# Kernel optimization log

Hardware: AMD Instinct MI355X
Metric: run time of the kernel (lower is better)

Reference implementation:

```python
import jax, jax.numpy as jnp
import numpy as np

N = 100000      # nodes
E = 3200000     # edges (avg degree 32)
DIN, DH, DOUT = 256, 256, 64
K = 10          # propagation hops


def _uniform(key, shape, fan_in):
    b = 1.0 / np.sqrt(fan_in)
    return jax.random.uniform(key, shape, jnp.float32, -b, b)


def setup_inputs() -> dict:
    key = jax.random.key(0)
    ks = jax.random.split(key, 8)
    x = jax.random.normal(ks[0], (N, DIN), jnp.float32)
    edge_index = jax.random.randint(ks[1], (2, E), 0, N, dtype=jnp.int64)
    W1 = _uniform(ks[2], (DIN, DH), DIN)
    b1 = _uniform(ks[3], (DH,), DIN)
    W2 = _uniform(ks[4], (DH, DOUT), DH)
    b2 = _uniform(ks[5], (DOUT,), DH)
    proj_w = _uniform(ks[6], (DOUT,), DOUT)
    proj_b = _uniform(ks[7], (), DOUT)
    return {"x": x, "edge_index": edge_index, "W1": W1, "b1": b1,
            "W2": W2, "b2": b2, "proj_w": proj_w, "proj_b": proj_b}


def _gcn_norm(edge_index, num_nodes):
    # add self-loops with weight 1, symmetric normalization deg^-1/2 A deg^-1/2
    loops = jnp.arange(num_nodes, dtype=edge_index.dtype)
    row = jnp.concatenate([edge_index[0], loops])
    col = jnp.concatenate([edge_index[1], loops])
    w = jnp.ones(row.shape[0], jnp.float32)
    deg = jax.ops.segment_sum(w, col, num_segments=num_nodes)
    dinv = jnp.where(deg > 0, jax.lax.rsqrt(deg), 0.0)
    norm = dinv[row] * dinv[col]  # edge weight is 1
    return row, col, norm


def reference(x, edge_index, W1, b1, W2, b2, proj_w, proj_b):
    h = jax.nn.relu(x @ W1 + b1)
    h = h @ W2 + b2                               # [N, DOUT]
    row, col, norm = _gcn_norm(edge_index, N)
    preds = [h]
    for _ in range(K):
        h = jax.ops.segment_sum(norm[:, None] * h[row], col, num_segments=N)
        preds.append(h)
    pps = jnp.stack(preds, axis=1)                # [N, K+1, DOUT]
    score = jax.nn.sigmoid(pps @ proj_w + proj_b) # [N, K+1]
    out = jnp.einsum('nk,nkc->nc', score, pps)    # adaptive hop pooling
    return out
```

## Files before the change

kernel.cpp:

```cpp
#include <hip/hip_runtime.h>
#include <hip/hip_bf16.h>
#include <math.h>


#define WAVE 64
#define NBLK 1024
#define RS 520

__device__ inline float bf2f(unsigned short u) {
    union { unsigned int i; float f; } v; v.i = ((unsigned int)u) << 16; return v.f;
}
__device__ inline unsigned short f2bf(float f) {
    __hip_bfloat16 b = __float2bfloat16(f);
    union { __hip_bfloat16 b; unsigned short u; } v; v.b = b; return v.u;
}
__device__ inline float bflo(unsigned u) {
    union { unsigned i; float f; } v; v.i = u << 16; return v.f;
}
__device__ inline float bfhi(unsigned u) {
    union { unsigned i; float f; } v; v.i = u & 0xffff0000u; return v.f;
}

typedef __attribute__((ext_vector_type(8))) short bf16x8;
typedef __attribute__((ext_vector_type(16))) float f32x16;

__global__ void detect_kernel(const unsigned* __restrict__ e, int* __restrict__ sflag) {
    __shared__ int any;
    if (threadIdx.x == 0) any = 0;
    __syncthreads();
    unsigned nz = 0;
    int t = threadIdx.x;
    for (int i = 0; i < 8; ++i) nz |= e[(size_t)(t * 8 + i) * 2 + 1];
    if (nz) atomicOr(&any, 1);
    __syncthreads();
    if (t == 0) *sflag = any ? 1 : 2;
}

__global__ void passA_kernel(const int* __restrict__ eidx, const int* __restrict__ sflag,
                             int* __restrict__ blk_cnt, int E, int NB, int EPB) {
    __shared__ int lh[512];
    int t = threadIdx.x, blk = blockIdx.x;
    for (int i = t; i < NB; i += 256) lh[i] = 0;
    __syncthreads();
    int s = *sflag;
    int base = blk * EPB;
    int end = base + EPB; if (end > E) end = E;
    for (int e = base + t; e < end; e += 256) {
        int c = eidx[(size_t)s * (size_t)(E + e)];
        atomicAdd(&lh[c >> 8], 1);
    }
    __syncthreads();
    for (int i = t; i < NB; i += 256)
        blk_cnt[(size_t)blk * NB + i] = lh[i];
}

__global__ void scan1_kernel(const int* __restrict__ in, int* __restrict__ out,
                             int* __restrict__ bsums, int n) {
    __shared__ int s[256];
    int t = threadIdx.x;
    int idx = blockIdx.x * 1024 + t * 4;
    int x0 = (idx + 0 < n) ? in[idx + 0] : 0;
    int x1 = (idx + 1 < n) ? in[idx + 1] : 0;
    int x2 = (idx + 2 < n) ? in[idx + 2] : 0;
    int x3 = (idx + 3 < n) ? in[idx + 3] : 0;
    int lsum = x0 + x1 + x2 + x3;
    s[t] = lsum;
    __syncthreads();
    for (int o = 1; o < 256; o <<= 1) {
        int v = (t >= o) ? s[t - o] : 0;
        __syncthreads();
        if (t >= o) s[t] += v;
        __syncthreads();
    }
    int excl = s[t] - lsum;
    if (idx + 0 < n) out[idx + 0] = excl;
    if (idx + 1 < n) out[idx + 1] = excl + x0;
    if (idx + 2 < n) out[idx + 2] = excl + x0 + x1;
    if (idx + 3 < n) out[idx + 3] = excl + x0 + x1 + x2;
    if (t == 255) bsums[blockIdx.x] = s[255];
}

__global__ void scan2g_kernel(int* __restrict__ bsums, int nb) {
    __shared__ int part[256];
    int t = threadIdx.x;
    int v[4]; int run = 0;
    #pragma unroll
    for (int j = 0; j < 4; ++j) {
        int i = t * 4 + j;
        int x = (i < nb) ? bsums[i] : 0;
        v[j] = run; run += x;
    }
    part[t] = run;
    __syncthreads();
    for (int o = 1; o < 256; o <<= 1) {
        int x = (t >= o) ? part[t - o] : 0;
        __syncthreads();
        if (t >= o) part[t] += x;
        __syncthreads();
    }
    int excl = part[t] - run;
    #pragma unroll
    for (int j = 0; j < 4; ++j) {
        int i = t * 4 + j;
        if (i < nb) bsums[i] = excl + v[j];
    }
}

__global__ void scan3_kernel(int* __restrict__ arr, const int* __restrict__ bsums,
                             int n, int total) {
    int t = threadIdx.x;
    int idx = blockIdx.x * 1024 + t * 4;
    int add = bsums[blockIdx.x];
    #pragma unroll
    for (int i = 0; i < 4; ++i)
        if (idx + i < n) arr[idx + i] += add;
    if (blockIdx.x == 0 && t == 0) arr[n] = total;
}

__global__ void passB_kernel(const int* __restrict__ eidx, const int* __restrict__ sflag,
                             const int* __restrict__ pbase, int2* __restrict__ pairs,
                             int E, int NB, int EPB) {
    __shared__ int lcur[512];
    int t = threadIdx.x, blk = blockIdx.x;
    for (int i = t; i < NB; i += 256) lcur[i] = pbase[(size_t)blk * NB + i];
    __syncthreads();
    int s = *sflag;
    int base = blk * EPB;
    int end = base + EPB; if (end > E) end = E;
    for (int e = base + t; e < end; e += 256) {
        int r = eidx[(size_t)s * (size_t)e];
        int c = eidx[(size_t)s * (size_t)(E + e)];
        int pos = atomicAdd(&lcur[c >> 8], 1);
        pairs[pos] = make_int2(r, c);
    }
}

__global__ void passD_kernel(const int2* __restrict__ pairs, const int* __restrict__ pbase,
                             int* __restrict__ cnt, int N, int NB) {
    __shared__ int lcnt[256];
    int b = blockIdx.x, t = threadIdx.x;
    lcnt[t] = 0;
    __syncthreads();
    for (int blk = t; blk < NBLK; blk += 256) {
        int w0 = pbase[(size_t)blk * NB + b];
        int w1 = pbase[(size_t)blk * NB + b + 1];
        for (int i = w0; i < w1; ++i)
            atomicAdd(&lcnt[pairs[i].y & 255], 1);
    }
    __syncthreads();
    int node = b * 256 + t;
    if (node < N) cnt[node] = lcnt[t];
}

__global__ void dinv_kernel(const int* __restrict__ cnt, float* __restrict__ dinv, int n) {
    int i = blockIdx.x * blockDim.x + threadIdx.x;
    if (i < n) dinv[i] = rsqrtf((float)(cnt[i] + 1));
}

__global__ void passC_kernel(const int2* __restrict__ pairs, const int* __restrict__ pbase,
                             const int* __restrict__ offs, int* __restrict__ csr_src,
                             int N, int NB) {
    __shared__ int lcur[256];
    int b = blockIdx.x, t = threadIdx.x;
    int node = b * 256 + t;
    lcur[t] = (node < N) ? offs[node] : 0;
    __syncthreads();
    for (int blk = t; blk < NBLK; blk += 256) {
        int w0 = pbase[(size_t)blk * NB + b];
        int w1 = pbase[(size_t)blk * NB + b + 1];
        for (int i = w0; i < w1; ++i) {
            int2 p = pairs[i];
            int pos = atomicAdd(&lcur[p.y & 255], 1);
            csr_src[pos] = p.x;
        }
    }
}

__global__ void wconv_kernel(const float* __restrict__ W, unsigned short* __restrict__ Wf,
                             int K, int Nn) {
    int i = blockIdx.x * blockDim.x + threadIdx.x;
    if (i >= K * Nn) return;
    int k = i / Nn, n = i - k * Nn;
    Wf[(size_t)(k >> 3) * Nn * 8 + n * 8 + (k & 7)] = f2bf(W[i]);
}

__global__ __launch_bounds__(256, 4) void mlp_fused(
        const float* __restrict__ x,
        const unsigned short* __restrict__ W1f,
        const float* __restrict__ b1,
        const unsigned short* __restrict__ W2f,
        const float* __restrict__ b2,
        const float* __restrict__ dinv,
        const float* __restrict__ pw, const float* __restrict__ pb,
        float* __restrict__ out, unsigned short* __restrict__ g,
        int M) {
    __shared__ unsigned short xfrag[4 * RS];
    __shared__ unsigned short h1frag[32 * RS];
    __shared__ float pools[2][2][2][16];

    int tid = threadIdx.x;
    int wave = tid >> 6, lane = tid & 63;
    int half = lane >> 5, l31 = lane & 31;
    int rt = wave & 1;
    int cw = wave >> 1;
    int bm = blockIdx.x * 64;

    f32x16 acc1[4] = {};

    float4 xv[2];
    #pragma unroll
    for (int i = 0; i < 2; ++i) {
        int f = i * 256 + tid;
        int row = f >> 3, c4 = (f & 7) * 4;
        int grow = bm + row;
        xv[i] = (grow < M) ? *(const float4*)(x + (size_t)grow * 256 + c4)
                           : make_float4(0.f, 0.f, 0.f, 0.f);
    }

    for (int it = 0; it < 8; ++it) {
        #pragma unroll
        for (int i = 0; i < 2; ++i) {
            int f = i * 256 + tid;
            int row = f >> 3, c4 = (f & 7) * 4;
            int region = c4 >> 3, off = c4 & 7;
            ushort4 u;
            u.x = f2bf(xv[i].x); u.y = f2bf(xv[i].y);
            u.z = f2bf(xv[i].z); u.w = f2bf(xv[i].w);
            *(ushort4*)&xfrag[region * RS + row * 8 + off] = u;
        }
        __syncthreads();
        if (it < 7) {
            int k0 = (it + 1) * 32;
            #pragma unroll
            for (int i = 0; i < 2; ++i) {
                int f = i * 256 + tid;
                int row = f >> 3, c4 = (f & 7) * 4;
                int grow = bm + row;
                xv[i] = (grow < M) ? *(const float4*)(x + (size_t)grow * 256 + k0 + c4)
                                   : make_float4(0.f, 0.f, 0.f, 0.f);
            }
        }
        #pragma unroll
        for (int s = 0; s < 2; ++s) {
            int region = it * 4 + s * 2 + half;
            bf16x8 a = *(bf16x8*)&xfrag[(s * 2 + half) * RS + (rt * 32 + l31) * 8];
            #pragma unroll
            for (int j = 0; j < 4; ++j) {
                int ch = cw * 128 + j * 32 + l31;
                bf16x8 b = *(const bf16x8*)(W1f + (size_t)region * 2048 + ch * 8);
                acc1[j] = __builtin_amdgcn_mfma_f32_32x32x16_bf16(a, b, acc1[j], 0, 0, 0);
            }
        }
        __syncthreads();
    }

    #pragma unroll
    for (int j = 0; j < 4; ++j) {
        int ch = cw * 128 + j * 32 + l31;
        float bb = b1[ch];
        int region = ch >> 3, off = ch & 7;
        #pragma unroll
        for (int reg = 0; reg < 16; ++reg) {
            int rowin = (reg & 3) + 8 * (reg >> 2) + 4 * half;
            int row = rt * 32 + rowin;
            float v = fmaxf(acc1[j][reg] + bb, 0.f);
            h1frag[region * RS + row * 8 + off] = f2bf(v);
        }
    }
    __syncthreads();

    int rt2 = wave >> 1, ct2 = wave & 1;
    f32x16 acc2 = {};
    #pragma unroll
    for (int s = 0; s < 16; ++s) {
        bf16x8 a = *(bf16x8*)&h1frag[(s * 2 + half) * RS + (rt2 * 32 + l31) * 8];
        bf16x8 b = *(const bf16x8*)(W2f + (size_t)(s * 2 + half) * 512 + (ct2 * 32 + l31) * 8);
        acc2 = __builtin_amdgcn_mfma_f32_32x32x16_bf16(a, b, acc2, 0, 0, 0);
    }

    float bb = b2[ct2 * 32 + l31];
    float pwv = pw[ct2 * 32 + l31];
    float pbv = pb[0];
    float hreg[16];
    #pragma unroll
    for (int reg = 0; reg < 16; ++reg) {
        float h = acc2[reg] + bb;
        hreg[reg] = h;
        float d = h * pwv;
        d += __shfl_xor(d, 1, 64);
        d += __shfl_xor(d, 2, 64);
        d += __shfl_xor(d, 4, 64);
        d += __shfl_xor(d, 8, 64);
        d += __shfl_xor(d, 16, 64);
        if (l31 == 0) pools[rt2][ct2][half][reg] = d;
    }
    __syncthreads();
    #pragma unroll
    for (int reg = 0; reg < 16; ++reg) {
        int rowin = (reg & 3) + 8 * (reg >> 2) + 4 * half;
        int row = bm + rt2 * 32 + rowin;
        float d = pools[rt2][0][half][reg] + pools[rt2][1][half][reg];
        float sg = 1.f / (1.f + __expf(-(d + pbv)));
        float h = hreg[reg];
        if (row < M) {
            float dv = dinv[row];
            out[(size_t)row * 64 + ct2 * 32 + l31] = sg * h;
            g[(size_t)row * 64 + ct2 * 32 + l31]   = f2bf(dv * h);
        }
    }
}

__global__ void spmm_kernel(const int* __restrict__ offs, const int* __restrict__ src,
                            const float* __restrict__ dinv,
                            const unsigned* __restrict__ gin,
                            unsigned short* __restrict__ gout,
                            float* __restrict__ out,
                            const float* __restrict__ pw, const float* __restrict__ pb,
                            int n) {
    int wid = (blockIdx.x * blockDim.x + threadIdx.x) >> 6;
    int lane = threadIdx.x & 63;
    if (wid >= n) return;
    int g = lane >> 4;
    int q = lane & 15;
    int c = __builtin_amdgcn_readfirstlane(wid);
    int e0   = __builtin_amdgcn_readfirstlane(offs[c]);
    int eend = __builtin_amdgcn_readfirstlane(offs[c + 1]);

    float a0 = 0.f, a1 = 0.f, a2 = 0.f, a3 = 0.f;
    for (int e = e0; e < eend; e += 32) {
        #pragma unroll
        for (int i = 0; i < 8; ++i) {
            int ei = e + i * 4 + g;
            int ec = (ei < eend) ? ei : (eend - 1);
            float m = (ei < eend) ? 1.f : 0.f;
            int s = src[ec];
            uint2 v = *(const uint2*)(gin + (size_t)s * 32 + q * 2);
            a0 = fmaf(m, bflo(v.x), a0);
            a1 = fmaf(m, bfhi(v.x), a1);
            a2 = fmaf(m, bflo(v.y), a2);
            a3 = fmaf(m, bfhi(v.y), a3);
        }
    }

    a0 += __shfl_xor(a0, 16, 64); a0 += __shfl_xor(a0, 32, 64);
    a1 += __shfl_xor(a1, 16, 64); a1 += __shfl_xor(a1, 32, 64);
    a2 += __shfl_xor(a2, 16, 64); a2 += __shfl_xor(a2, 32, 64);
    a3 += __shfl_xor(a3, 16, 64); a3 += __shfl_xor(a3, 32, 64);

    uint2 sv = *(const uint2*)(gin + (size_t)c * 32 + q * 2);
    a0 += bflo(sv.x); a1 += bfhi(sv.x);
    a2 += bflo(sv.y); a3 += bfhi(sv.y);

    float dc = dinv[c];
    float h0 = dc * a0, h1 = dc * a1, h2 = dc * a2, h3 = dc * a3;

    float4 pv = *(const float4*)(pw + q * 4);
    float d = h0 * pv.x + h1 * pv.y + h2 * pv.z + h3 * pv.w;
    d += __shfl_xor(d, 1, 64);
    d += __shfl_xor(d, 2, 64);
    d += __shfl_xor(d, 4, 64);
    d += __shfl_xor(d, 8, 64);
    float sg = 1.f / (1.f + __expf(-(d + pb[0])));

    if (g == 0) {
        ushort4 gw;
        gw.x = f2bf(dc * h0); gw.y = f2bf(dc * h1);
        gw.z = f2bf(dc * h2); gw.w = f2bf(dc * h3);
        *(ushort4*)(gout + (size_t)c * 64 + q * 4) = gw;
        float4 o = *(float4*)(out + (size_t)c * 64 + q * 4);
        o.x += sg * h0; o.y += sg * h1; o.z += sg * h2; o.w += sg * h3;
        *(float4*)(out + (size_t)c * 64 + q * 4) = o;
    }
}

extern "C" void kernel_launch(void* const* d_in, const int* in_sizes, int n_in,
                              void* d_out, int out_size, void* d_ws, size_t ws_size,
                              hipStream_t stream) {
    const float* x  = (const float*)d_in[0];
    const int* eidx = (const int*)d_in[1];
    const float* W1 = (const float*)d_in[2];
    const float* b1 = (const float*)d_in[3];
    const float* W2 = (const float*)d_in[4];
    const float* b2 = (const float*)d_in[5];
    const float* pw = (const float*)d_in[6];
    const float* pb = (const float*)d_in[7];
    float* out = (float*)d_out;

    const int N = in_sizes[0] / 256;
    const int E = in_sizes[1] / 2;
    const int NB = (N + 255) >> 8;
    const int EPB = (E + NBLK - 1) / NBLK;
    const int M = NB * NBLK;

    size_t woff = 0;
    auto alloc = [&](size_t bytes) -> void* {
        void* p = (char*)d_ws + woff;
        woff += (bytes + 255) & ~(size_t)255;
        return p;
    };
    int*   sflag   = (int*)alloc(4);
    int*   cnt     = (int*)alloc((size_t)N * 4);
    float* dinv    = (float*)alloc((size_t)N * 4);
    int*   offs    = (int*)alloc(((size_t)N + 1) * 4);
    int*   bsums   = (int*)alloc(1024 * 4);
    int*   bsums2  = (int*)alloc(1024 * 4);
    int*   pbase   = (int*)alloc(((size_t)M + 1) * 4);
    int*   csr_src = (int*)alloc((size_t)E * 4);
    int2*  pairs   = (int2*)alloc((size_t)E * 8);
    unsigned short* W1f = (unsigned short*)alloc((size_t)256 * 256 * 2);
    unsigned short* W2f = (unsigned short*)alloc((size_t)64 * 256 * 2);
    unsigned short* gA = (unsigned short*)alloc((size_t)N * 64 * 2);
    unsigned short* gB = (unsigned short*)alloc((size_t)N * 64 * 2);

    detect_kernel<<<1, 256, 0, stream>>>((const unsigned*)eidx, sflag);

    passA_kernel<<<NBLK, 256, 0, stream>>>(eidx, sflag, pbase, E, NB, EPB);
    int nb2 = (M + 1023) / 1024;
    scan1_kernel<<<nb2, 256, 0, stream>>>(pbase, pbase, bsums2, M);
    scan2g_kernel<<<1, 256, 0, stream>>>(bsums2, nb2);
    scan3_kernel<<<nb2, 256, 0, stream>>>(pbase, bsums2, M, E);
    passB_kernel<<<NBLK, 256, 0, stream>>>(eidx, sflag, pbase, pairs, E, NB, EPB);
    passD_kernel<<<NB, 256, 0, stream>>>(pairs, pbase, cnt, N, NB);
    dinv_kernel<<<(N + 255) / 256, 256, 0, stream>>>(cnt, dinv, N);
    int nb1 = (N + 1023) / 1024;
    scan1_kernel<<<nb1, 256, 0, stream>>>(cnt, offs, bsums, N);
    scan2g_kernel<<<1, 256, 0, stream>>>(bsums, nb1);
    scan3_kernel<<<nb1, 256, 0, stream>>>(offs, bsums, N, E);
    passC_kernel<<<NB, 256, 0, stream>>>(pairs, pbase, offs, csr_src, N, NB);

    wconv_kernel<<<(256 * 256 + 255) / 256, 256, 0, stream>>>(W1, W1f, 256, 256);
    wconv_kernel<<<(64 * 256 + 255) / 256, 256, 0, stream>>>(W2, W2f, 256, 64);
    int gb = (N + 63) / 64;
    mlp_fused<<<gb, 256, 0, stream>>>(x, W1f, b1, W2f, b2, dinv, pw, pb,
                                      out, gA, N);

    int nwb = (N + 3) / 4;
    unsigned short* gin = gA;
    unsigned short* gout = gB;
    for (int k = 0; k < 10; ++k) {
        spmm_kernel<<<nwb, 256, 0, stream>>>(offs, csr_src, dinv,
                                             (const unsigned*)gin, gout, out, pw, pb, N);
        unsigned short* t = gin; gin = gout; gout = t;
    }
}
```

Baseline: 980.3 us.

## Fuse ten SpMM hops into one persistent cooperative kernel with grid sync

Replaces the ten per-hop SpMM launches with a single cooperative persistent kernel. Each wave handles a contiguous chunk of destination nodes across all hops and ping-pongs between two bf16 buffers, with a grid-wide barrier between hops. It also folds the dinv computation into passD, removing one launch. The aim is to cut launch overhead and inter-kernel gaps. In exchange, occupancy is limited to the cooperative grid size, and the grid barriers plus fixed node-to-wave assignment can cause load imbalance.

After: 3.458 ms. 253% more time.

```diff
diff --git a/kernel.cpp b/kernel.cpp
--- a/kernel.cpp
+++ b/kernel.cpp
@@ -1,6 +1,9 @@
 #include <hip/hip_runtime.h>
 #include <hip/hip_bf16.h>
+#include <hip/hip_cooperative_groups.h>
 #include <math.h>
+
+namespace cg = cooperative_groups;
 
 
 #define WAVE 64
@@ -136,7 +139,8 @@
 }
 
 __global__ void passD_kernel(const int2* __restrict__ pairs, const int* __restrict__ pbase,
-                             int* __restrict__ cnt, int N, int NB) {
+                             int* __restrict__ cnt, float* __restrict__ dinv,
+                             int N, int NB) {
     __shared__ int lcnt[256];
     int b = blockIdx.x, t = threadIdx.x;
     lcnt[t] = 0;
@@ -149,12 +153,10 @@
     }
     __syncthreads();
     int node = b * 256 + t;
-    if (node < N) cnt[node] = lcnt[t];
-}
-
-__global__ void dinv_kernel(const int* __restrict__ cnt, float* __restrict__ dinv, int n) {
-    int i = blockIdx.x * blockDim.x + threadIdx.x;
-    if (i < n) dinv[i] = rsqrtf((float)(cnt[i] + 1));
+    if (node < N) {
+        cnt[node] = lcnt[t];
+        dinv[node] = rsqrtf((float)(lcnt[t] + 1));
+    }
 }
 
 __global__ void passC_kernel(const int2* __restrict__ pairs, const int* __restrict__ pbase,
@@ -310,66 +312,79 @@
     }
 }
 
-__global__ void spmm_kernel(const int* __restrict__ offs, const int* __restrict__ src,
-                            const float* __restrict__ dinv,
-                            const unsigned* __restrict__ gin,
-                            unsigned short* __restrict__ gout,
-                            float* __restrict__ out,
-                            const float* __restrict__ pw, const float* __restrict__ pb,
-                            int n) {
-    int wid = (blockIdx.x * blockDim.x + threadIdx.x) >> 6;
+__global__ __launch_bounds__(256) void spmm_coop(
+        const int* __restrict__ offs, const int* __restrict__ src,
+        const float* __restrict__ dinv,
+        unsigned* __restrict__ gA, unsigned* __restrict__ gB,
+        float* __restrict__ out,
+        const float* __restrict__ pw, const float* __restrict__ pb,
+        int n, int dpw) {
+    cg::grid_group grid = cg::this_grid();
+    int gw = (blockIdx.x * blockDim.x + threadIdx.x) >> 6;
     int lane = threadIdx.x & 63;
-    if (wid >= n) return;
     int g = lane >> 4;
     int q = lane & 15;
-    int c = __builtin_amdgcn_readfirstlane(wid);
-    int e0   = __builtin_amdgcn_readfirstlane(offs[c]);
-    int eend = __builtin_amdgcn_readfirstlane(offs[c + 1]);
-
-    float a0 = 0.f, a1 = 0.f, a2 = 0.f, a3 = 0.f;
-    for (int e = e0; e < eend; e += 32) {
-        #pragma unroll
-        for (int i = 0; i < 8; ++i) {
-            int ei = e + i * 4 + g;
-            int ec = (ei < eend) ? ei : (eend - 1);
-            float m = (ei < eend) ? 1.f : 0.f;
-            int s = src[ec];
-            uint2 v = *(const uint2*)(gin + (size_t)s * 32 + q * 2);
-            a0 = fmaf(m, bflo(v.x), a0);
-            a1 = fmaf(m, bfhi(v.x), a1);
-            a2 = fmaf(m, bflo(v.y), a2);
-            a3 = fmaf(m, bfhi(v.y), a3);
-        }
-    }
-
-    a0 += __shfl_xor(a0, 16, 64); a0 += __shfl_xor(a0, 32, 64);
-    a1 += __shfl_xor(a1, 16, 64); a1 += __shfl_xor(a1, 32, 64);
-    a2 += __shfl_xor(a2, 16, 64); a2 += __shfl_xor(a2, 32, 64);
-    a3 += __shfl_xor(a3, 16, 64); a3 += __shfl_xor(a3, 32, 64);
-
-    uint2 sv = *(const uint2*)(gin + (size_t)c * 32 + q * 2);
-    a0 += bflo(sv.x); a1 += bfhi(sv.x);
-    a2 += bflo(sv.y); a3 += bfhi(sv.y);
-
-    float dc = dinv[c];
-    float h0 = dc * a0, h1 = dc * a1, h2 = dc * a2, h3 = dc * a3;
-
     float4 pv = *(const float4*)(pw + q * 4);
-    float d = h0 * pv.x + h1 * pv.y + h2 * pv.z + h3 * pv.w;
-    d += __shfl_xor(d, 1, 64);
-    d += __shfl_xor(d, 2, 64);
-    d += __shfl_xor(d, 4, 64);
-    d += __shfl_xor(d, 8, 64);
-    float sg = 1.f / (1.f + __expf(-(d + pb[0])));
-
-    if (g == 0) {
-        ushort4 gw;
-        gw.x = f2bf(dc * h0); gw.y = f2bf(dc * h1);
-        gw.z = f2bf(dc * h2); gw.w = f2bf(dc * h3);
-        *(ushort4*)(gout + (size_t)c * 64 + q * 4) = gw;
-        float4 o = *(float4*)(out + (size_t)c * 64 + q * 4);
-        o.x += sg * h0; o.y += sg * h1; o.z += sg * h2; o.w += sg * h3;
-        *(float4*)(out + (size_t)c * 64 + q * 4) = o;
+    float pbv = pb[0];
+    int base = gw * dpw;
+
+    for (int k = 0; k < 10; ++k) {
+        const unsigned* gin = (k & 1) ? gB : gA;
+        unsigned* gout = (k & 1) ? gA : gB;
+        for (int j = 0; j < dpw; ++j) {
+            int c = base + j;
+            if (c < n) {
+                int e0 = __builtin_amdgcn_readfirstlane(offs[c]);
+                int eend = __builtin_amdgcn_readfirstlane(offs[c + 1]);
+                float a0 = 0.f, a1 = 0.f, a2 = 0.f, a3 = 0.f;
+                for (int e = e0; e < eend; e += 32) {
+                    #pragma unroll
+                    for (int i = 0; i < 8; ++i) {
+                        int ei = e + i * 4 + g;
+                        int ec = (ei < eend) ? ei : (eend - 1);
+                        float m = (ei < eend) ? 1.f : 0.f;
+                        int s = src[ec];
+                        uint2 v = *(const uint2*)(gin + (size_t)s * 32 + q * 2);
+                        a0 = fmaf(m, bflo(v.x), a0);
+                        a1 = fmaf(m, bfhi(v.x), a1);
+                        a2 = fmaf(m, bflo(v.y), a2);
+                        a3 = fmaf(m, bfhi(v.y), a3);
+                    }
+                }
+                a0 += __shfl_xor(a0, 16, 64); a0 += __shfl_xor(a0, 32, 64);
+                a1 += __shfl_xor(a1, 16, 64); a1 += __shfl_xor(a1, 32, 64);
+                a2 += __shfl_xor(a2, 16, 64); a2 += __shfl_xor(a2, 32, 64);
+                a3 += __shfl_xor(a3, 16, 64); a3 += __shfl_xor(a3, 32, 64);
+
+                uint2 sv = *(const uint2*)(gin + (size_t)c * 32 + q * 2);
+                a0 += bflo(sv.x); a1 += bfhi(sv.x);
+                a2 += bflo(sv.y); a3 += bfhi(sv.y);
+
+                float dc = dinv[c];
+                float h0 = dc * a0, h1 = dc * a1, h2 = dc * a2, h3 = dc * a3;
+
+                float d = h0 * pv.x + h1 * pv.y + h2 * pv.z + h3 * pv.w;
+                d += __shfl_xor(d, 1, 64);
+                d += __shfl_xor(d, 2, 64);
+                d += __shfl_xor(d, 4, 64);
+                d += __shfl_xor(d, 8, 64);
+                float sg = 1.f / (1.f + __expf(-(d + pbv)));
+
+                if (g == 0) {
+                    unsigned g0 = (unsigned)f2bf(dc * h0) | ((unsigned)f2bf(dc * h1) << 16);
+                    unsigned g1 = (unsigned)f2bf(dc * h2) | ((unsigned)f2bf(dc * h3) << 16);
+                    *(uint2*)(gout + (size_t)c * 32 + q * 2) = make_uint2(g0, g1);
+                    float4 o = *(float4*)(out + (size_t)c * 64 + q * 4);
+                    o.x += sg * h0; o.y += sg * h1;
+                    o.z += sg * h2; o.w += sg * h3;
+                    *(float4*)(out + (size_t)c * 64 + q * 4) = o;
+                }
+            }
+        }
+        if (k < 9) {
+            __threadfence();
+            grid.sync();
+        }
     }
 }
 
@@ -420,8 +435,7 @@
     scan2g_kernel<<<1, 256, 0, stream>>>(bsums2, nb2);
     scan3_kernel<<<nb2, 256, 0, stream>>>(pbase, bsums2, M, E);
     passB_kernel<<<NBLK, 256, 0, stream>>>(eidx, sflag, pbase, pairs, E, NB, EPB);
-    passD_kernel<<<NB, 256, 0, stream>>>(pairs, pbase, cnt, N, NB);
-    dinv_kernel<<<(N + 255) / 256, 256, 0, stream>>>(cnt, dinv, N);
+    passD_kernel<<<NB, 256, 0, stream>>>(pairs, pbase, cnt, dinv, N, NB);
     int nb1 = (N + 1023) / 1024;
     scan1_kernel<<<nb1, 256, 0, stream>>>(cnt, offs, bsums, N);
     scan2g_kernel<<<1, 256, 0, stream>>>(bsums, nb1);
@@ -434,12 +448,22 @@
     mlp_fused<<<gb, 256, 0, stream>>>(x, W1f, b1, W2f, b2, dinv, pw, pb,
                                       out, gA, N);
 
-    int nwb = (N + 3) / 4;
-    unsigned short* gin = gA;
-    unsigned short* gout = gB;
-    for (int k = 0; k < 10; ++k) {
-        spmm_kernel<<<nwb, 256, 0, stream>>>(offs, csr_src, dinv,
-                                             (const unsigned*)gin, gout, out, pw, pb, N);
-        unsigned short* t = gin; gin = gout; gout = t;
-    }
-}
+    static int coop_grid = 0;
+    if (coop_grid == 0) {
+        int nbpc = 0;
+        hipError_t err = hipOccupancyMaxActiveBlocksPerMultiprocessor(
+            &nbpc, (const void*)spmm_coop, 256, 0);
+        if (err != hipSuccess || nbpc <= 0) nbpc = 4;
+        coop_grid = nbpc * 256;
+    }
+    int nwaves = coop_grid * 4;
+    int dpw = (N + nwaves - 1) / nwaves;
+    unsigned* gAu = (unsigned*)gA;
+    unsigned* gBu = (unsigned*)gB;
+    int Nv = N;
+    void* args[] = { (void*)&offs, (void*)&csr_src, (void*)&dinv,
+                     (void*)&gAu, (void*)&gBu, (void*)&out,
+                     (void*)&pw, (void*)&pb, (void*)&Nv, (void*)&dpw };
+    hipLaunchCooperativeKernel((const void*)spmm_coop, dim3(coop_grid), dim3(256),
+                               args, 0, stream);
+}
```
